# Performance work log

Hardware: AMD Instinct MI355X
Metric: run time of the kernel (lower is better)

The kernel has to match this reference:

```python
import jax, jax.numpy as jnp
import numpy as np

DIM = 256  # channel width
B, H, W = 4, 64, 64


def conv2d(x, w, b, pad, groups=1):
    # x: NCHW, w: OIHW (I = C_in/groups)
    y = jax.lax.conv_general_dilated(
        x, w, window_strides=(1, 1),
        padding=[(pad[0], pad[0]), (pad[1], pad[1])],
        dimension_numbers=("NCHW", "OIHW", "NCHW"),
        feature_group_count=groups)
    return y + b[None, :, None, None]


def l2norm(x, eps=1e-12):
    # matches F.normalize(x, dim=-1): x / max(||x||_2, eps)
    n = jnp.sqrt(jnp.sum(x * x, axis=-1, keepdims=True))
    return x / jnp.maximum(n, eps)


def setup_inputs() -> dict:
    key = jax.random.key(0)
    ks = jax.random.split(key, 12)
    dim, c8 = DIM, DIM // 8
    w = lambda k, shape, s: jax.random.normal(k, shape, jnp.float32) * s
    return {
        "x": jax.random.normal(ks[0], (B, dim, H, W), jnp.float32),
        "w_conv": w(ks[1], (dim, dim, 3, 3), 0.02), "b_conv": jnp.zeros((dim,), jnp.float32),
        "w01": w(ks[2], (dim, 1, 1, 7), 0.05), "b01": jnp.zeros((dim,), jnp.float32),
        "w02": w(ks[3], (dim, 1, 7, 1), 0.05), "b02": jnp.zeros((dim,), jnp.float32),
        "w11": w(ks[4], (dim, 1, 1, 11), 0.05), "b11": jnp.zeros((dim,), jnp.float32),
        "w12": w(ks[5], (dim, 1, 11, 1), 0.05), "b12": jnp.zeros((dim,), jnp.float32),
        "w21": w(ks[6], (dim, 1, 1, 21), 0.05), "b21": jnp.zeros((dim,), jnp.float32),
        "w22": w(ks[7], (dim, 1, 21, 1), 0.05), "b22": jnp.zeros((dim,), jnp.float32),
        "w_proj": w(ks[8], (c8, dim, 1, 1), 0.05), "b_proj": jnp.zeros((c8,), jnp.float32),
        "w3": w(ks[9], (c8, dim // 4, 1, 1), 0.05), "b3": jnp.zeros((c8,), jnp.float32),
        "w4": w(ks[10], (dim, c8, 1, 1), 0.05), "b4": jnp.zeros((dim,), jnp.float32),
    }


def reference(x, w_conv, b_conv, w01, b01, w02, b02, w11, b11, w12, b12,
              w21, b21, w22, b22, w_proj, b_proj, w3, b3, w4, b4):
    b, c, h, w_ = x.shape
    x = conv2d(x, w_conv, b_conv, (1, 1))
    # multi-scale separable depthwise convs (7, 11, 21)
    x1 = conv2d(conv2d(x, w01, b01, (0, 3), c), w02, b02, (3, 0), c)
    x2 = conv2d(conv2d(x, w11, b11, (0, 5), c), w12, b12, (5, 0), c)
    x3 = conv2d(conv2d(x, w21, b21, (0, 10), c), w22, b22, (10, 0), c)
    out1 = x1 + x2 + x3 + x                      # [b, dim, h, w]
    out1 = conv2d(out1, w_proj, b_proj, (0, 0))  # [b, dim//8, h, w]
    c8 = out1.shape[1]
    t = out1.reshape(b, c8, h * w_)              # b head c (h w), head=1

    q1 = l2norm(t)
    attn1 = jax.nn.softmax(q1 @ jnp.swapaxes(q1, -2, -1), axis=-1)  # [b, c8, c8]
    out2 = attn1 @ t                                                # [b, c8, hw]

    # branch 2: spatial attention (hw x hw)
    ts = jnp.swapaxes(t, -2, -1)                 # [b, hw, c8]
    q2 = l2norm(ts)
    attn2 = jax.nn.softmax(q2 @ jnp.swapaxes(q2, -2, -1), axis=-1)  # [b, hw, hw]
    out3 = jnp.swapaxes(attn2 @ ts, -2, -1)                         # [b, c8, hw]

    out4 = jnp.concatenate([out2.reshape(b, c8, h, w_),
                            out3.reshape(b, c8, h, w_)], axis=1)    # [b, dim//4, h, w]
    out5 = conv2d(out4, w3, b3, (0, 0)) + out1
    return conv2d(out5, w4, b4, (0, 0))          # [b, dim, h, w]
```

## Files before the change

### kernel.cpp

```cpp
#include <hip/hip_runtime.h>
#include <hip/hip_bf16.h>

typedef __hip_bfloat16 bf16;
typedef short s16;
typedef __attribute__((ext_vector_type(4))) short s16x4;
typedef __attribute__((ext_vector_type(8))) short s16x8;
typedef __attribute__((ext_vector_type(4))) float f32x4;

__device__ __forceinline__ s16 f2b(float f){
    unsigned u = __float_as_uint(f);
    unsigned r = (u + 0x7FFFu + ((u >> 16) & 1u)) >> 16;
    return (s16)r;
}
__device__ __forceinline__ float b2f_bits(s16 v){
    return __uint_as_float(((unsigned)(unsigned short)v) << 16);
}

__global__ __launch_bounds__(256) void prep_k(const float* __restrict__ x, s16* __restrict__ xcl,
                                              const float* __restrict__ w, s16* __restrict__ wpk){
    __shared__ s16 lb[64][258];
    int blk = blockIdx.x, t = threadIdx.x;
    if (blk < 256){
        int h = blk & 63, b = blk >> 6;
        for (int i = t; i < 16384; i += 256){
            int ci = i >> 6, ww = i & 63;
            lb[ww][ci] = f2b(x[((b*256 + ci)*64 + h)*64 + ww]);
        }
        __syncthreads();
        for (int i = t; i < 16384; i += 256){
            int ww = i >> 8, ci = i & 255;
            xcl[(b*4096 + h*64 + ww)*256 + ci] = lb[ww][ci];
        }
    } else {
        int base = (blk - 256)*1024 + t;
        #pragma unroll
        for (int k = 0; k < 4; ++k){
            int idx = base + k*256;
            int cil = idx & 31;
            int r   = idx >> 5;
            int co  = r & 255;
            int r2  = r >> 8;
            int tap = r2 % 9, cc = r2 / 9;
            wpk[idx] = f2b(w[(co*256 + cc*32 + cil)*9 + tap]);
        }
    }
}

__global__ __launch_bounds__(256) void conv3x3m_k(const s16* __restrict__ xcl,
        const s16* __restrict__ wpk, const float* __restrict__ bias,
        bf16* __restrict__ y0){
    __shared__ alignas(16) s16 smem[30240];
    s16* xls = smem;
    s16* wls = smem + 9504;
    const int sp = blockIdx.x, cog = blockIdx.y;
    const int b = sp >> 5, h0 = (sp & 31)*2;
    const int t = threadIdx.x;
    const int wv = t >> 6, lane = t & 63;
    const int lm = lane & 15, g = lane >> 4;

    f32x4 acc[2][4];
    #pragma unroll
    for (int mi = 0; mi < 2; ++mi)
        #pragma unroll
        for (int ni = 0; ni < 4; ++ni) acc[mi][ni] = (f32x4){0.f,0.f,0.f,0.f};

    for (int cc = 0; cc < 8; ++cc){
        __syncthreads();
        for (int i = t; i < 1056; i += 256){
            int g8 = i & 3, wi = (i>>2) % 66, r = (i>>2) / 66;
            int h = h0 - 1 + r, w = wi - 1;
            s16x8 v = {0,0,0,0,0,0,0,0};
            if (h >= 0 && h < 64 && w >= 0 && w < 64)
                v = *(const s16x8*)&xcl[(b*4096 + h*64 + w)*256 + cc*32 + g8*8];
            s16* d = &xls[(r*66 + wi)*36 + g8*8];
            *(s16x4*)d       = __builtin_shufflevector(v, v, 0,1,2,3);
            *(s16x4*)(d + 4) = __builtin_shufflevector(v, v, 4,5,6,7);
        }
        for (int i = t; i < 2304; i += 256){
            int g8 = i & 3, co = (i>>2) & 63, tap = i >> 8;
            s16x8 v = *(const s16x8*)&wpk[((cc*9 + tap)*256 + cog*64 + co)*32 + g8*8];
            s16* d = &wls[(tap*64 + co)*36 + g8*8];
            *(s16x4*)d       = __builtin_shufflevector(v, v, 0,1,2,3);
            *(s16x4*)(d + 4) = __builtin_shufflevector(v, v, 4,5,6,7);
        }
        __syncthreads();
        #pragma unroll
        for (int tap = 0; tap < 9; ++tap){
            const int kh = tap/3, kw = tap%3;
            s16x8 bfr[4], afr[2];
            #pragma unroll
            for (int ni = 0; ni < 4; ++ni){
                const s16* p = &wls[(tap*64 + ni*16 + lm)*36 + g*8];
                s16x4 lo = *(const s16x4*)p;
                s16x4 hi = *(const s16x4*)(p + 4);
                bfr[ni] = __builtin_shufflevector(lo, hi, 0,1,2,3,4,5,6,7);
            }
            #pragma unroll
            for (int mi = 0; mi < 2; ++mi){
                int m = (wv*2 + mi)*16 + lm;
                int hr = m >> 6, ww = m & 63;
                const s16* p = &xls[((hr + kh)*66 + (ww + kw))*36 + g*8];
                s16x4 lo = *(const s16x4*)p;
                s16x4 hi = *(const s16x4*)(p + 4);
                afr[mi] = __builtin_shufflevector(lo, hi, 0,1,2,3,4,5,6,7);
            }
            #pragma unroll
            for (int mi = 0; mi < 2; ++mi)
                #pragma unroll
                for (int ni = 0; ni < 4; ++ni)
                    acc[mi][ni] = __builtin_amdgcn_mfma_f32_16x16x32_bf16(
                        afr[mi], bfr[ni], acc[mi][ni], 0, 0, 0);
        }
    }
    __syncthreads();
    float* ot = (float*)smem;
    #pragma unroll
    for (int mi = 0; mi < 2; ++mi)
        #pragma unroll
        for (int ni = 0; ni < 4; ++ni)
            #pragma unroll
            for (int r = 0; r < 4; ++r){
                int m  = (wv*2 + mi)*16 + g*4 + r;
                int co = ni*16 + lm;
                ot[co*132 + m] = acc[mi][ni][r];
            }
    __syncthreads();
    for (int i = t; i < 8192; i += 256){
        int co = i >> 7, m = i & 127;
        float v = ot[co*132 + m] + bias[cog*64 + co];
        y0[((b*256 + cog*64 + co)*64 + h0 + (m>>6))*64 + (m & 63)] = __float2bfloat16(v);
    }
}

template<int K>
__device__ __forceinline__ void sep_branch(const float (*__restrict__ pl)[65], float (*__restrict__ hp)[65],
                                           int c, int t,
                                           const float* __restrict__ wh, const float* __restrict__ bh,
                                           const float* __restrict__ wv, const float* __restrict__ bv,
                                           float* acc){
    constexpr int P = K/2;
    constexpr int W = 16 + 2*P;
    float wk[K];
    #pragma unroll
    for (int j = 0; j < K; ++j) wk[j] = wh[c*K + j];
    float bhv = bh[c];
    {
        int h = t >> 2, w0 = (t & 3)*16;
        float win[W];
        #pragma unroll
        for (int j = 0; j < W; ++j){
            int ww = w0 - P + j;
            win[j] = (ww >= 0 && ww < 64) ? pl[h][ww] : 0.f;
        }
        __syncthreads();
        #pragma unroll
        for (int i = 0; i < 16; ++i){
            float s = bhv;
            #pragma unroll
            for (int k = 0; k < K; ++k) s += win[i+k]*wk[k];
            hp[h][w0 + i] = s;
        }
    }
    float vk[K];
    #pragma unroll
    for (int j = 0; j < K; ++j) vk[j] = wv[c*K + j];
    float bvv = bv[c];
    __syncthreads();
    {
        int w = t & 63, h0 = (t >> 6)*16;
        float win[W];
        #pragma unroll
        for (int j = 0; j < W; ++j){
            int hh = h0 - P + j;
            win[j] = (hh >= 0 && hh < 64) ? hp[hh][w] : 0.f;
        }
        #pragma unroll
        for (int i = 0; i < 16; ++i){
            float s = bvv;
            #pragma unroll
            for (int k = 0; k < K; ++k) s += win[i+k]*vk[k];
            acc[i] += s;
        }
    }
}

__global__ __launch_bounds__(256) void sepconv_k(const bf16* __restrict__ y0,
        const float* __restrict__ w01, const float* __restrict__ b01,
        const float* __restrict__ w02, const float* __restrict__ b02,
        const float* __restrict__ w11, const float* __restrict__ b11,
        const float* __restrict__ w12, const float* __restrict__ b12,
        const float* __restrict__ w21, const float* __restrict__ b21,
        const float* __restrict__ w22, const float* __restrict__ b22,
        bf16* __restrict__ out1){
    __shared__ float pl[64][65];
    __shared__ float hp[64][65];
    int bc = blockIdx.x;
    int c = bc & 255;
    int t = threadIdx.x;
    const bf16* src = y0 + bc*4096;
    for (int i = t; i < 4096; i += 256) pl[i>>6][i&63] = __bfloat162float(src[i]);
    __syncthreads();
    float acc[16];
    #pragma unroll
    for (int k = 0; k < 16; ++k) acc[k] = 0.f;
    sep_branch<7 >(pl, hp, c, t, w01, b01, w02, b02, acc);
    sep_branch<11>(pl, hp, c, t, w11, b11, w12, b12, acc);
    sep_branch<21>(pl, hp, c, t, w21, b21, w22, b22, acc);
    bf16* dst = out1 + bc*4096;
    {
        int w = t & 63, h0 = (t >> 6)*16;
        #pragma unroll
        for (int i = 0; i < 16; ++i)
            dst[(h0 + i)*64 + w] = __float2bfloat16(acc[i] + pl[h0 + i][w]);
    }
}

__global__ __launch_bounds__(256) void proj_k(const bf16* __restrict__ out1, const float* __restrict__ wp,
                                              const float* __restrict__ bp,
                                              s16* __restrict__ tTb, float* __restrict__ rn2){
    __shared__ float wl[256*32];
    __shared__ s16 part[4][64][36];
    int pt = blockIdx.x, b = blockIdx.y, t = threadIdx.x;
    int q = t >> 6, lane = t & 63;
    for (int i = t; i < 8192; i += 256){
        int ci = i >> 5, cc = i & 31;
        wl[ci*32 + cc] = wp[cc*256 + ci];
    }
    __syncthreads();
    int p = pt*64 + lane;
    float acc[32] = {};
    const bf16* xb = out1 + b*1048576 + p;
    for (int ci = q*64; ci < q*64 + 64; ++ci){
        float v = __bfloat162float(xb[ci*4096]);
        const float* wr = &wl[ci*32];
        #pragma unroll
        for (int c8 = 0; c8 < 8; ++c8){
            float4 w4 = *(const float4*)&wr[c8*4];
            acc[c8*4+0] += w4.x*v; acc[c8*4+1] += w4.y*v;
            acc[c8*4+2] += w4.z*v; acc[c8*4+3] += w4.w*v;
        }
    }
    #pragma unroll
    for (int cc = 0; cc < 32; ++cc) part[q][lane][cc] = f2b(acc[cc]);
    __syncthreads();
    int p_loc = t >> 2, qq = t & 3;
    int pg = pt*64 + p_loc;
    float a8[8];
    float ss = 0.f;
    #pragma unroll
    for (int c = 0; c < 8; ++c){
        int cc = qq*8 + c;
        float v = b2f_bits(part[0][p_loc][cc]) + b2f_bits(part[1][p_loc][cc])
                + b2f_bits(part[2][p_loc][cc]) + b2f_bits(part[3][p_loc][cc]) + bp[cc];
        a8[c] = v;
        ss += v*v;
    }
    ss += __shfl_xor(ss, 1, 4);
    ss += __shfl_xor(ss, 2, 4);
    if (qq == 0) rn2[b*4096 + pg] = 1.f / fmaxf(sqrtf(ss), 1e-12f);
    s16x8 o8;
    #pragma unroll
    for (int c = 0; c < 8; ++c) o8[c] = f2b(a8[c]);
    *(s16x8*)&tTb[(b*4096 + pg)*32 + qq*8] = o8;
}

__global__ __launch_bounds__(256) void gramm_k(const s16* __restrict__ tTb, float* __restrict__ part){
    __shared__ alignas(16) s16 ts[32*268];
    int ks = blockIdx.x, b = blockIdx.y, t = threadIdx.x;
    {
        const s16* src = &tTb[(b*4096 + ks*256 + t)*32];
        s16 row[32];
        #pragma unroll
        for (int q = 0; q < 4; ++q){
            s16x8 v = *(const s16x8*)&src[q*8];
            #pragma unroll
            for (int e = 0; e < 8; ++e) row[q*8 + e] = v[e];
        }
        #pragma unroll
        for (int cc = 0; cc < 32; ++cc) ts[cc*268 + t] = row[cc];
    }
    __syncthreads();
    int wv = t >> 6, lane = t & 63, lm = lane & 15, g = lane >> 4;
    int mi = wv >> 1, ni = wv & 1;
    f32x4 acc = (f32x4){0.f,0.f,0.f,0.f};
    const s16* ar = &ts[(mi*16 + lm)*268];
    const s16* br = &ts[(ni*16 + lm)*268];
    #pragma unroll
    for (int kk = 0; kk < 8; ++kk){
        const s16* ap = ar + kk*32 + g*8;
        s16x4 alo = *(const s16x4*)ap;
        s16x4 ahi = *(const s16x4*)(ap + 4);
        s16x8 af = __builtin_shufflevector(alo, ahi, 0,1,2,3,4,5,6,7);
        const s16* bp = br + kk*32 + g*8;
        s16x4 blo = *(const s16x4*)bp;
        s16x4 bhi = *(const s16x4*)(bp + 4);
        s16x8 bf = __builtin_shufflevector(blo, bhi, 0,1,2,3,4,5,6,7);
        acc = __builtin_amdgcn_mfma_f32_16x16x32_bf16(af, bf, acc, 0, 0, 0);
    }
    float* pd = part + (b*16 + ks)*1024;
    #pragma unroll
    for (int r = 0; r < 4; ++r){
        int i = mi*16 + g*4 + r, j = ni*16 + lm;
        pd[i*32 + j] = acc[r];
    }
}

__global__ __launch_bounds__(256) void afold_k(const float* __restrict__ part,
        const float* __restrict__ w3, const float* __restrict__ b3,
        const float* __restrict__ w4, const float* __restrict__ b4,
        float* __restrict__ WtT, float* __restrict__ WoT, float* __restrict__ bfo){
    __shared__ float rn[32];
    __shared__ float rsum[32];
    __shared__ float a1[1024];
    __shared__ float w3a[1024];
    __shared__ float w3bs[1024];
    int b = blockIdx.x, t = threadIdx.x;
    if (t < 32){
        float gjj = 0.f;
        #pragma unroll 8
        for (int ps = 0; ps < 16; ++ps) gjj += part[(b*16+ps)*1024 + t*33];
        rn[t] = 1.f / fmaxf(sqrtf(gjj), 1e-12f);
    }
    for (int idx = t; idx < 1024; idx += 256){
        int i = idx >> 5, j = idx & 31;
        w3bs[idx] = w3[i*64 + 32 + j];
    }
    __syncthreads();
    for (int e = t; e < 1024; e += 256){
        int i = e >> 5, j = e & 31;
        float gij = 0.f;
        #pragma unroll 8
        for (int ps = 0; ps < 16; ++ps) gij += part[(b*16+ps)*1024 + e];
        a1[e] = __expf(rn[i]*rn[j]*gij);
    }
    __syncthreads();
    if (t < 32){
        float s = 0.f;
        #pragma unroll 8
        for (int j = 0; j < 32; ++j) s += a1[t*32 + j];
        rsum[t] = 1.f / s;
    }
    __syncthreads();
    for (int e = t; e < 1024; e += 256) a1[e] *= rsum[e >> 5];
    __syncthreads();
    for (int idx = t; idx < 1024; idx += 256){
        int cc = idx >> 5, j = idx & 31;
        float s = 0.f;
        #pragma unroll 8
        for (int i = 0; i < 32; ++i) s += w3[cc*64 + i]*a1[i*32 + j];
        w3a[idx] = s;
    }
    __syncthreads();
    int co = t;
    float w4r[32];
    #pragma unroll
    for (int cc = 0; cc < 32; ++cc) w4r[cc] = w4[co*32 + cc];
    float bfv = b4[co];
    #pragma unroll
    for (int cc = 0; cc < 32; ++cc) bfv += w4r[cc]*b3[cc];
    bfo[b*256 + co] = bfv;
    for (int j = 0; j < 32; ++j){
        float st = w4r[j];
        float so = 0.f;
        #pragma unroll 8
        for (int cc = 0; cc < 32; ++cc){
            st += w4r[cc]*w3a[cc*32 + j];
            so += w4r[cc]*w3bs[cc*32 + j];
        }
        WtT[(b*32 + j)*256 + co] = st;
        WoT[(b*32 + j)*256 + co] = so;
    }
}

__global__ __launch_bounds__(256) void flashm_k(const s16* __restrict__ tTb, const float* __restrict__ rn2,
                                                float* __restrict__ partA, float* __restrict__ partL){
    __shared__ alignas(16) s16 kvb[128*36];
    __shared__ alignas(16) s16 vts[32*132];
    __shared__ alignas(16) s16 pls[4][16*132];
    __shared__ float rnj[128];
    __shared__ float ri[64];
    const int ib = blockIdx.x, b = blockIdx.y, chunk = blockIdx.z;
    const int t = threadIdx.x, wv = t >> 6, lane = t & 63;
    const int lm = lane & 15, g = lane >> 4;
    const int i0 = ib*64;

    if (t < 64) ri[t] = rn2[b*4096 + i0 + t];
    s16x8 qf = *(const s16x8*)&tTb[(b*4096 + i0 + wv*16 + lm)*32 + g*8];
    __syncthreads();
    float rni4[4];
    #pragma unroll
    for (int r = 0; r < 4; ++r) rni4[r] = ri[wv*16 + g*4 + r];

    f32x4 oacc[2];
    oacc[0] = (f32x4){0.f,0.f,0.f,0.f};
    oacc[1] = (f32x4){0.f,0.f,0.f,0.f};
    float lacc[4] = {0.f,0.f,0.f,0.f};
    s16* pw = pls[wv];

    for (int jt = chunk*8; jt < chunk*8 + 8; ++jt){
        const int j0 = jt*128;
        __syncthreads();
        for (int gi = t; gi < 512; gi += 256){
            int j = gi >> 2, g8 = gi & 3;
            s16x8 v = *(const s16x8*)&tTb[(b*4096 + j0 + j)*32 + g8*8];
            s16* d = &kvb[j*36 + g8*8];
            *(s16x4*)d       = __builtin_shufflevector(v, v, 0,1,2,3);
            *(s16x4*)(d + 4) = __builtin_shufflevector(v, v, 4,5,6,7);
            #pragma unroll
            for (int e = 0; e < 8; ++e) vts[(g8*8 + e)*132 + j] = v[e];
        }
        if (t < 128) rnj[t] = rn2[b*4096 + j0 + t];
        __syncthreads();
        #pragma unroll
        for (int nt = 0; nt < 8; ++nt){
            const s16* bp = &kvb[(nt*16 + lm)*36 + g*8];
            s16x4 blo = *(const s16x4*)bp;
            s16x4 bhi = *(const s16x4*)(bp + 4);
            s16x8 bf = __builtin_shufflevector(blo, bhi, 0,1,2,3,4,5,6,7);
            f32x4 s = __builtin_amdgcn_mfma_f32_16x16x32_bf16(qf, bf,
                        (f32x4){0.f,0.f,0.f,0.f}, 0, 0, 0);
            float rj = rnj[nt*16 + lm];
            #pragma unroll
            for (int r = 0; r < 4; ++r){
                float e = __expf(s[r]*rni4[r]*rj);
                lacc[r] += e;
                pw[(g*4 + r)*132 + nt*16 + lm] = f2b(e);
            }
        }
        #pragma unroll
        for (int ks = 0; ks < 4; ++ks){
            const s16* ap = &pw[lm*132 + ks*32 + g*8];
            s16x4 alo = *(const s16x4*)ap;
            s16x4 ahi = *(const s16x4*)(ap + 4);
            s16x8 af = __builtin_shufflevector(alo, ahi, 0,1,2,3,4,5,6,7);
            #pragma unroll
            for (int n2 = 0; n2 < 2; ++n2){
                const s16* vp = &vts[(n2*16 + lm)*132 + ks*32 + g*8];
                s16x4 vlo = *(const s16x4*)vp;
                s16x4 vhi = *(const s16x4*)(vp + 4);
                s16x8 vf = __builtin_shufflevector(vlo, vhi, 0,1,2,3,4,5,6,7);
                oacc[n2] = __builtin_amdgcn_mfma_f32_16x16x32_bf16(af, vf, oacc[n2], 0, 0, 0);
            }
        }
    }
    #pragma unroll
    for (int r = 0; r < 4; ++r){
        float v = lacc[r];
        v += __shfl_xor(v, 1, 16); v += __shfl_xor(v, 2, 16);
        v += __shfl_xor(v, 4, 16); v += __shfl_xor(v, 8, 16);
        lacc[r] = v;
    }
    const int base = (b*4 + chunk)*4096 + i0 + wv*16;
    #pragma unroll
    for (int n2 = 0; n2 < 2; ++n2)
        #pragma unroll
        for (int r = 0; r < 4; ++r)
            partA[(base + g*4 + r)*32 + n2*16 + lm] = oacc[n2][r];
    if (lm == 0){
        #pragma unroll
        for (int r = 0; r < 4; ++r) partL[base + g*4 + r] = lacc[r];
    }
}

__global__ __launch_bounds__(256) void finalfuse_k(const s16* __restrict__ tTb,
        const float* __restrict__ partA, const float* __restrict__ partL,
        const float* __restrict__ WtT, const float* __restrict__ WoT,
        const float* __restrict__ bfo, float* __restrict__ out){
    int pt = blockIdx.x, cog = blockIdx.y, b = blockIdx.z, t = threadIdx.x;
    int p = pt*256 + t;
    float l = 0.f;
    #pragma unroll
    for (int c = 0; c < 4; ++c) l += partL[(b*4 + c)*4096 + p];
    float inv = 1.f / l;
    float v3[32];
    #pragma unroll
    for (int q = 0; q < 8; ++q){
        float4 s0 = *(const float4*)&partA[((b*4 + 0)*4096 + p)*32 + q*4];
        float4 s1 = *(const float4*)&partA[((b*4 + 1)*4096 + p)*32 + q*4];
        float4 s2 = *(const float4*)&partA[((b*4 + 2)*4096 + p)*32 + q*4];
        float4 s3 = *(const float4*)&partA[((b*4 + 3)*4096 + p)*32 + q*4];
        v3[q*4+0] = (s0.x + s1.x + s2.x + s3.x)*inv;
        v3[q*4+1] = (s0.y + s1.y + s2.y + s3.y)*inv;
        v3[q*4+2] = (s0.z + s1.z + s2.z + s3.z)*inv;
        v3[q*4+3] = (s0.w + s1.w + s2.w + s3.w)*inv;
    }
    float vt[32];
    {
        const s16* tp = &tTb[(b*4096 + p)*32];
        #pragma unroll
        for (int q = 0; q < 4; ++q){
            s16x8 v = *(const s16x8*)&tp[q*8];
            #pragma unroll
            for (int e = 0; e < 8; ++e) vt[q*8 + e] = b2f_bits(v[e]);
        }
    }
    float acc[32];
    #pragma unroll
    for (int co = 0; co < 32; ++co) acc[co] = bfo[b*256 + cog*32 + co];
    for (int j = 0; j < 32; ++j){
        float vtj = vt[j];
        float vo  = v3[j];
        const float* wtr = WtT + (b*32 + j)*256 + cog*32;
        const float* wor = WoT + (b*32 + j)*256 + cog*32;
        #pragma unroll
        for (int co = 0; co < 32; ++co) acc[co] += wtr[co]*vtj + wor[co]*vo;
    }
    #pragma unroll
    for (int co = 0; co < 32; ++co)
        out[((b*256 + cog*32 + co)*4096) + p] = acc[co];
}

extern "C" void kernel_launch(void* const* d_in, const int* in_sizes, int n_in,
                              void* d_out, int out_size, void* d_ws, size_t ws_size,
                              hipStream_t stream) {
    const float* x      = (const float*)d_in[0];
    const float* w_conv = (const float*)d_in[1];
    const float* b_conv = (const float*)d_in[2];
    const float* w01 = (const float*)d_in[3];  const float* b01 = (const float*)d_in[4];
    const float* w02 = (const float*)d_in[5];  const float* b02 = (const float*)d_in[6];
    const float* w11 = (const float*)d_in[7];  const float* b11 = (const float*)d_in[8];
    const float* w12 = (const float*)d_in[9];  const float* b12 = (const float*)d_in[10];
    const float* w21 = (const float*)d_in[11]; const float* b21 = (const float*)d_in[12];
    const float* w22 = (const float*)d_in[13]; const float* b22 = (const float*)d_in[14];
    const float* w_proj = (const float*)d_in[15]; const float* b_proj = (const float*)d_in[16];
    const float* w3 = (const float*)d_in[17]; const float* b3 = (const float*)d_in[18];
    const float* w4 = (const float*)d_in[19]; const float* b4 = (const float*)d_in[20];

    char* wsb = (char*)d_ws;
    s16*   xcl  = (s16*)wsb;
    bf16*  out1 = (bf16*)wsb;
    bf16*  y0   = (bf16*)(wsb + 8388608);
    s16*   wpk  = (s16*)(wsb + 16777216);
    float* f    = (float*)d_ws;
    float* part   = f + 0;
    float* partA  = f + 0;
    s16*   tTb    = (s16*)(wsb + 10485760);
    float* WtT    = f + 3145728;
    float* WoT    = f + 3178496;
    float* bfo    = f + 3211264;
    float* partL  = f + 4194304;
    float* rn2    = f + 4726912;

    prep_k<<<dim3(832), 256, 0, stream>>>(x, xcl, w_conv, wpk);
    conv3x3m_k<<<dim3(128, 4), 256, 0, stream>>>(xcl, wpk, b_conv, y0);
    sepconv_k<<<dim3(1024), 256, 0, stream>>>(y0, w01, b01, w02, b02,
                                              w11, b11, w12, b12,
                                              w21, b21, w22, b22, out1);
    proj_k<<<dim3(64, 4), 256, 0, stream>>>(out1, w_proj, b_proj, tTb, rn2);
    gramm_k<<<dim3(16, 4), 256, 0, stream>>>(tTb, part);
    afold_k<<<dim3(4), 256, 0, stream>>>(part, w3, b3, w4, b4, WtT, WoT, bfo);
    flashm_k<<<dim3(64, 4, 4), 256, 0, stream>>>(tTb, rn2, partA, partL);
    finalfuse_k<<<dim3(16, 8, 4), 256, 0, stream>>>(tTb, partA, partL, WtT, WoT, bfo,
                                                    (float*)d_out);
}
```

Baseline: 294.7 us.

## Load conv3x3 activation fragments directly from global instead of LDS staging

The 3x3 conv kernel no longer stages the input halo tile in shared memory. Each wave now reads its A fragments straight from global memory (relying on L1/L2 for reuse across the 9 taps), and the weight tile uses 16-byte stores and loads with a 40-element row pitch. This removes the LDS fill and its share of shared memory, which may raise occupancy. In exchange it issues 9x redundant global loads per fragment with boundary checks inside the MFMA loop, which can expose latency.

After: 306.7 us. 1.04x slower.

```diff
diff --git a/kernel.cpp b/kernel.cpp
--- a/kernel.cpp
+++ b/kernel.cpp
@@ -49,9 +49,7 @@
 __global__ __launch_bounds__(256) void conv3x3m_k(const s16* __restrict__ xcl,
         const s16* __restrict__ wpk, const float* __restrict__ bias,
         bf16* __restrict__ y0){
-    __shared__ alignas(16) s16 smem[30240];
-    s16* xls = smem;
-    s16* wls = smem + 9504;
+    __shared__ alignas(16) s16 smem[23040];
     const int sp = blockIdx.x, cog = blockIdx.y;
     const int b = sp >> 5, h0 = (sp & 31)*2;
     const int t = threadIdx.x;
@@ -64,24 +62,15 @@
         #pragma unroll
         for (int ni = 0; ni < 4; ++ni) acc[mi][ni] = (f32x4){0.f,0.f,0.f,0.f};
 
+    int hr0 = ((wv*2 + 0)*16 + lm) >> 6, ww0 = ((wv*2 + 0)*16 + lm) & 63;
+    int hr1 = ((wv*2 + 1)*16 + lm) >> 6, ww1 = ((wv*2 + 1)*16 + lm) & 63;
+
     for (int cc = 0; cc < 8; ++cc){
         __syncthreads();
-        for (int i = t; i < 1056; i += 256){
-            int g8 = i & 3, wi = (i>>2) % 66, r = (i>>2) / 66;
-            int h = h0 - 1 + r, w = wi - 1;
-            s16x8 v = {0,0,0,0,0,0,0,0};
-            if (h >= 0 && h < 64 && w >= 0 && w < 64)
-                v = *(const s16x8*)&xcl[(b*4096 + h*64 + w)*256 + cc*32 + g8*8];
-            s16* d = &xls[(r*66 + wi)*36 + g8*8];
-            *(s16x4*)d       = __builtin_shufflevector(v, v, 0,1,2,3);
-            *(s16x4*)(d + 4) = __builtin_shufflevector(v, v, 4,5,6,7);
-        }
         for (int i = t; i < 2304; i += 256){
             int g8 = i & 3, co = (i>>2) & 63, tap = i >> 8;
             s16x8 v = *(const s16x8*)&wpk[((cc*9 + tap)*256 + cog*64 + co)*32 + g8*8];
-            s16* d = &wls[(tap*64 + co)*36 + g8*8];
-            *(s16x4*)d       = __builtin_shufflevector(v, v, 0,1,2,3);
-            *(s16x4*)(d + 4) = __builtin_shufflevector(v, v, 4,5,6,7);
+            *(s16x8*)&smem[(tap*64 + co)*40 + g8*8] = v;
         }
         __syncthreads();
         #pragma unroll
@@ -89,20 +78,21 @@
             const int kh = tap/3, kw = tap%3;
             s16x8 bfr[4], afr[2];
             #pragma unroll
-            for (int ni = 0; ni < 4; ++ni){
-                const s16* p = &wls[(tap*64 + ni*16 + lm)*36 + g*8];
-                s16x4 lo = *(const s16x4*)p;
-                s16x4 hi = *(const s16x4*)(p + 4);
-                bfr[ni] = __builtin_shufflevector(lo, hi, 0,1,2,3,4,5,6,7);
+            for (int ni = 0; ni < 4; ++ni)
+                bfr[ni] = *(const s16x8*)&smem[(tap*64 + ni*16 + lm)*40 + g*8];
+            {
+                int hh = h0 + hr0 + kh - 1, ww = ww0 + kw - 1;
+                s16x8 v = {0,0,0,0,0,0,0,0};
+                if ((unsigned)hh < 64u && (unsigned)ww < 64u)
+                    v = *(const s16x8*)&xcl[(b*4096 + hh*64 + ww)*256 + cc*32 + g*8];
+                afr[0] = v;
             }
-            #pragma unroll
-            for (int mi = 0; mi < 2; ++mi){
-                int m = (wv*2 + mi)*16 + lm;
-                int hr = m >> 6, ww = m & 63;
-                const s16* p = &xls[((hr + kh)*66 + (ww + kw))*36 + g*8];
-                s16x4 lo = *(const s16x4*)p;
-                s16x4 hi = *(const s16x4*)(p + 4);
-                afr[mi] = __builtin_shufflevector(lo, hi, 0,1,2,3,4,5,6,7);
+            {
+                int hh = h0 + hr1 + kh - 1, ww = ww1 + kw - 1;
+                s16x8 v = {0,0,0,0,0,0,0,0};
+                if ((unsigned)hh < 64u && (unsigned)ww < 64u)
+                    v = *(const s16x8*)&xcl[(b*4096 + hh*64 + ww)*256 + cc*32 + g*8];
+                afr[1] = v;
             }
             #pragma unroll
             for (int mi = 0; mi < 2; ++mi)
```
